# Kernel optimization log

Measured on AMD Instinct MI355X. Metric: run time of the kernel, lower is better.

The kernel has to match this reference:

```python
import jax, jax.numpy as jnp
import numpy as np

N = 8000          # num_nodes
DEG = 8           # avg out-degree of random road graph
B = 32            # batch size
INPUT_DIM = 2
UNITS = 64        # rnn_units
K = 2             # max_diffusion_step
NUM_SUPPORTS = 2  # dual_random_walk


def _spmm(rows, cols, vals, x):
    # sparse @ dense: y[r] += vals * x[c] for each coo entry (r, c)
    return jax.ops.segment_sum(vals[:, None] * x[cols], rows, num_segments=N)


def _gconv(inputs, state, supports, W, b):
    # Chebyshev-style diffusion conv, faithful to GCONV.forward layout
    Bsz = inputs.shape[0]
    x = jnp.concatenate([inputs.reshape(Bsz, N, -1), state.reshape(Bsz, N, -1)], axis=2)
    F = x.shape[2]                                   # input_dim + units
    x0 = jnp.transpose(x, (1, 2, 0)).reshape(N, F * Bsz)
    xs = [x0]
    for rows, cols, vals in supports:
        x1 = _spmm(rows, cols, vals, x0)
        xs.append(x1)
        xk2, xk1 = x0, x1
        for _ in range(2, K + 1):
            x2 = 2.0 * _spmm(rows, cols, vals, xk1) - xk2
            xs.append(x2)
            xk2, xk1 = xk1, x2
    M = len(xs)                                      # num_matrices = 2*K+1
    xc = jnp.stack(xs).reshape(M, N, F, Bsz)
    xc = jnp.transpose(xc, (3, 1, 2, 0)).reshape(Bsz * N, F * M)
    out = xc @ W + b
    return out.reshape(Bsz, N * W.shape[1])


def setup_inputs() -> dict:
    rng = np.random.default_rng(0)
    rows = np.repeat(np.arange(N, dtype=np.int32), DEG)
    cols = rng.integers(0, N, size=N * DEG).astype(np.int32)
    vals = rng.uniform(0.5, 1.5, size=N * DEG).astype(np.float32)
    # random-walk normalization: rw(A) = D^-1 A ; supports are rw(A).T and rw(A.T).T
    rsum = np.zeros(N, np.float32); np.add.at(rsum, rows, vals)
    csum = np.zeros(N, np.float32); np.add.at(csum, cols, vals)
    rinv = np.where(rsum > 0, 1.0 / np.maximum(rsum, 1e-12), 0.0).astype(np.float32)
    cinv = np.where(csum > 0, 1.0 / np.maximum(csum, 1e-12), 0.0).astype(np.float32)
    # support0 = (D^-1 A)^T: entry (cols[i], rows[i]) = vals[i] * rinv[rows[i]]
    s0_rows, s0_cols, s0_vals = cols, rows, (vals * rinv[rows]).astype(np.float32)
    # support1 = (D_T^-1 A^T)^T: entry (rows[i], cols[i]) = vals[i] * cinv[cols[i]]
    s1_rows, s1_cols, s1_vals = rows, cols, (vals * cinv[cols]).astype(np.float32)

    key = jax.random.key(0)
    k1, k2, k3, k4 = jax.random.split(key, 4)
    F = INPUT_DIM + UNITS
    M = NUM_SUPPORTS * K + 1
    xavier = lambda k, shape: jax.random.normal(k, shape, jnp.float32) * np.float32(np.sqrt(2.0 / (shape[0] + shape[1])))
    W_ru = xavier(k1, (F * M, 2 * UNITS))
    b_ru = jnp.ones((2 * UNITS,), jnp.float32)    # bias_start=1.0
    W_c = xavier(k2, (F * M, UNITS))
    b_c = jnp.zeros((UNITS,), jnp.float32)        # bias_start=0.0
    inputs = jax.random.normal(k3, (B, N * INPUT_DIM), jnp.float32)
    hx = jax.random.normal(k4, (B, N * UNITS), jnp.float32)
    return {
        "inputs": inputs, "hx": hx,
        "W_ru": W_ru, "b_ru": b_ru, "W_c": W_c, "b_c": b_c,
        "s0_rows": jnp.asarray(s0_rows), "s0_cols": jnp.asarray(s0_cols), "s0_vals": jnp.asarray(s0_vals),
        "s1_rows": jnp.asarray(s1_rows), "s1_cols": jnp.asarray(s1_cols), "s1_vals": jnp.asarray(s1_vals),
    }


def reference(inputs, hx, W_ru, b_ru, W_c, b_c,
              s0_rows, s0_cols, s0_vals, s1_rows, s1_cols, s1_vals):
    supports = [(s0_rows, s0_cols, s0_vals), (s1_rows, s1_cols, s1_vals)]
    value = jax.nn.sigmoid(_gconv(inputs, hx, supports, W_ru, b_ru))
    value = value.reshape(-1, N, 2 * UNITS)
    r = value[..., :UNITS].reshape(-1, N * UNITS)
    u = value[..., UNITS:].reshape(-1, N * UNITS)
    c = jnp.tanh(_gconv(inputs, r * hx, supports, W_c, b_c))
    return u * hx + (1.0 - u) * c
```

## Files before the change

### kernel.cpp

```cpp
#include <hip/hip_runtime.h>
#include <stdint.h>

typedef unsigned short u16;
typedef unsigned int   u32;

typedef __attribute__((ext_vector_type(8))) short bf16x8;
typedef __attribute__((ext_vector_type(4))) float f32x4;

#define NNODES 8000
#define BSZ    32
#define UNITS  64
#define EDG    64000
#define ROWCH  288
#define NODECH 1440
#define NODEU16 11520
#define KLIN   384
#define NSTEPS 12
#define HXROW  512000
#define INROW  16000

__device__ __forceinline__ u32 f2bf(float f){
    u32 u = __float_as_uint(f);
    return (u + 0x7FFFu + ((u >> 16) & 1u)) >> 16;
}
__device__ __forceinline__ float bfu(u16 s){ return __uint_as_float(((u32)s) << 16); }
__device__ __forceinline__ float lo16(u32 u){ return __uint_as_float(u << 16); }
__device__ __forceinline__ float hi16(u32 u){ return __uint_as_float(u & 0xFFFF0000u); }
__device__ __forceinline__ float sigm(float x){ return 1.f / (1.f + __expf(-x)); }

#define GLDS(gsrc, ldst) \
    __builtin_amdgcn_global_load_lds((const __attribute__((address_space(1))) void*)(gsrc), \
                                     (__attribute__((address_space(3))) void*)(ldst), 16, 0, 0)

__global__ void hist_k(const int* __restrict__ rows, int* __restrict__ counts){
    int e = blockIdx.x * 256 + threadIdx.x;
    if (e < EDG) atomicAdd(&counts[rows[e]], 1);
}

__global__ __launch_bounds__(256) void scan_k(const int* __restrict__ counts,
                                              int* __restrict__ row_ptr,
                                              int* __restrict__ cursor){
    __shared__ int part[256];
    int t = threadIdx.x;
    int s = 0;
    for (int i = 0; i < 32; ++i){ int r = t*32 + i; if (r < NNODES) s += counts[r]; }
    part[t] = s;
    __syncthreads();
    if (t == 0){
        int run = 0;
        for (int i = 0; i < 256; ++i){ int v = part[i]; part[i] = run; run += v; }
    }
    __syncthreads();
    int run = part[t];
    for (int i = 0; i < 32; ++i){
        int r = t*32 + i;
        if (r < NNODES){ row_ptr[r] = run; cursor[r] = run; run += counts[r]; }
    }
    if (t == 255) row_ptr[NNODES] = run;
}

__global__ void scatter_k(const int* __restrict__ rows, const int* __restrict__ cols,
                          const float* __restrict__ vals, int* __restrict__ cursor,
                          int* __restrict__ cs, float* __restrict__ vs){
    int e = blockIdx.x * 256 + threadIdx.x;
    if (e < EDG){
        int r = rows[e];
        int slot = atomicAdd(&cursor[r], 1);
        cs[slot] = cols[e];
        vs[slot] = vals[e];
    }
}

__global__ void prep_w_k(const float* __restrict__ W_ru, const float* __restrict__ W_c,
                         u16* __restrict__ Wt_ru, u16* __restrict__ Wt_c){
    int id = blockIdx.x * 256 + threadIdx.x;
    if (id < 128*KLIN){
        int j = id & 7;
        int cell = id >> 3;
        int col = cell & 127;
        int sq = cell >> 7;
        int kl = sq*8 + j;
        int m = kl / 72, fp = kl - m*72;
        u16 v = 0;
        if (m < 5 && fp < 66){
            float w;
            if (m == 0)      w = W_ru[(fp*5 + 0)*128 + col] - W_ru[(fp*5 + 2)*128 + col] - W_ru[(fp*5 + 4)*128 + col];
            else if (m == 2) w = 2.f * W_ru[(fp*5 + 2)*128 + col];
            else if (m == 4) w = 2.f * W_ru[(fp*5 + 4)*128 + col];
            else             w = W_ru[(fp*5 + m)*128 + col];
            v = (u16)f2bf(w);
        }
        Wt_ru[id] = v;
    }
    int id2 = id - 128*KLIN;
    if (id2 >= 0 && id2 < 64*KLIN){
        int j = id2 & 7;
        int cell = id2 >> 3;
        int col = cell & 63;
        int sq = cell >> 6;
        int kl = sq*8 + j;
        int m = kl / 72, fp = kl - m*72;
        u16 v = 0;
        if (m < 5 && fp < 66){
            float w;
            if (m == 0)      w = W_c[(fp*5 + 0)*64 + col] - W_c[(fp*5 + 2)*64 + col] - W_c[(fp*5 + 4)*64 + col];
            else if (m == 2) w = 2.f * W_c[(fp*5 + 2)*64 + col];
            else if (m == 4) w = 2.f * W_c[(fp*5 + 4)*64 + col];
            else             w = W_c[(fp*5 + m)*64 + col];
            v = (u16)f2bf(w);
        }
        Wt_c[id2] = v;
    }
}

__global__ __launch_bounds__(256) void build_x0_k(const float* __restrict__ inputs,
                                                  const float* __restrict__ hx,
                                                  u16* __restrict__ Xu){
    __shared__ float sl[32*72];
    int n = blockIdx.x, t = threadIdx.x;
    #pragma unroll
    for (int i = 0; i < 8; ++i){
        int idx = t + i*256;
        int b = idx >> 6, f = idx & 63;
        sl[b*72 + 2 + f] = hx[b*HXROW + n*64 + f];
    }
    if (t < 64){
        int b = t >> 1, d = t & 1;
        sl[b*72 + d] = inputs[b*INROW + n*2 + d];
    }
    if (t < 192){
        int b = t / 6, k = t - b*6;
        sl[b*72 + 66 + k] = 0.f;
    }
    __syncthreads();
    #pragma unroll
    for (int i = 0; i < 2; ++i){
        int j = t + i*256;
        if (j < ROWCH){
            int b = j & 31, s = j >> 5;
            const float* p = &sl[b*72 + s*8];
            uint4 o;
            o.x = f2bf(p[0]) | (f2bf(p[1]) << 16);
            o.y = f2bf(p[2]) | (f2bf(p[3]) << 16);
            o.z = f2bf(p[4]) | (f2bf(p[5]) << 16);
            o.w = f2bf(p[6]) | (f2bf(p[7]) << 16);
            ((uint4*)Xu)[(size_t)n*NODECH + j] = o;
        }
    }
}

__device__ __forceinline__ void acc8(float* a, uint4 q, float v){
    a[0] += v*lo16(q.x); a[1] += v*hi16(q.x);
    a[2] += v*lo16(q.y); a[3] += v*hi16(q.y);
    a[4] += v*lo16(q.z); a[5] += v*hi16(q.z);
    a[6] += v*lo16(q.w); a[7] += v*hi16(q.w);
}
__device__ __forceinline__ uint4 pack8(const float* a){
    uint4 o;
    o.x = f2bf(a[0]) | (f2bf(a[1]) << 16);
    o.y = f2bf(a[2]) | (f2bf(a[3]) << 16);
    o.z = f2bf(a[4]) | (f2bf(a[5]) << 16);
    o.w = f2bf(a[6]) | (f2bf(a[7]) << 16);
    return o;
}

__global__ __launch_bounds__(288) void diff1_k(u16* __restrict__ Xu,
                                               const int* __restrict__ rp,
                                               const int* __restrict__ c0, const float* __restrict__ v0,
                                               const int* __restrict__ c1, const float* __restrict__ v1){
    int t = threadIdx.x;
    if (t >= ROWCH) return;
    int n = blockIdx.x;
    const uint4* xb = (const uint4*)Xu;
    float a[8] = {0,0,0,0,0,0,0,0};
    float d[8] = {0,0,0,0,0,0,0,0};
    {
        uint4 q[8]; float vv[8];
        #pragma unroll
        for (int i = 0; i < 8; ++i){
            int c = c1[n*8 + i]; vv[i] = v1[n*8 + i];
            q[i] = xb[(size_t)c*NODECH + t];
        }
        #pragma unroll
        for (int i = 0; i < 8; ++i) acc8(d, q[i], vv[i]);
    }
    int e = rp[n], end = rp[n+1];
    for (; e + 8 <= end; e += 8){
        uint4 q[8]; float vv[8];
        #pragma unroll
        for (int i = 0; i < 8; ++i){
            int c = c0[e+i]; vv[i] = v0[e+i];
            q[i] = xb[(size_t)c*NODECH + t];
        }
        #pragma unroll
        for (int i = 0; i < 8; ++i) acc8(a, q[i], vv[i]);
    }
    for (; e < end; ++e){
        int c = c0[e]; float v = v0[e];
        acc8(a, xb[(size_t)c*NODECH + t], v);
    }
    ((uint4*)Xu)[(size_t)n*NODECH + 1*ROWCH + t] = pack8(a);
    ((uint4*)Xu)[(size_t)n*NODECH + 3*ROWCH + t] = pack8(d);
}

__global__ __launch_bounds__(288) void diff2_k(u16* __restrict__ Xu,
                                               const int* __restrict__ rp,
                                               const int* __restrict__ c0, const float* __restrict__ v0,
                                               const int* __restrict__ c1, const float* __restrict__ v1){
    int t = threadIdx.x;
    if (t >= ROWCH) return;
    int n = blockIdx.x;
    const uint4* xb = (const uint4*)Xu;
    float a[8] = {0,0,0,0,0,0,0,0};
    float d[8] = {0,0,0,0,0,0,0,0};
    {
        uint4 q[8]; float vv[8];
        #pragma unroll
        for (int i = 0; i < 8; ++i){
            int c = c1[n*8 + i]; vv[i] = v1[n*8 + i];
            q[i] = xb[(size_t)c*NODECH + 3*ROWCH + t];
        }
        #pragma unroll
        for (int i = 0; i < 8; ++i) acc8(d, q[i], vv[i]);
    }
    int e = rp[n], end = rp[n+1];
    for (; e + 8 <= end; e += 8){
        uint4 q[8]; float vv[8];
        #pragma unroll
        for (int i = 0; i < 8; ++i){
            int c = c0[e+i]; vv[i] = v0[e+i];
            q[i] = xb[(size_t)c*NODECH + 1*ROWCH + t];
        }
        #pragma unroll
        for (int i = 0; i < 8; ++i) acc8(a, q[i], vv[i]);
    }
    for (; e < end; ++e){
        int c = c0[e]; float v = v0[e];
        acc8(a, xb[(size_t)c*NODECH + 1*ROWCH + t], v);
    }
    ((uint4*)Xu)[(size_t)n*NODECH + 2*ROWCH + t] = pack8(a);
    ((uint4*)Xu)[(size_t)n*NODECH + 4*ROWCH + t] = pack8(d);
}

__global__ __launch_bounds__(1024) void gemm_ru_k(
        const u16* Xu,
        const u16* __restrict__ WtS,
        const float* __restrict__ b_ru,
        u16* __restrict__ U, u16* X0st){
    __shared__ u16 Bs[24576];
    const int t = threadIdx.x;
    const int lane = t & 63, w = t >> 6;
    const int node = blockIdx.x*16 + w;
    const int cIn = lane & 15, q = lane >> 4;
    const size_t noff = (size_t)node * NODEU16;
    const u16* Xn = Xu + noff;

    f32x4 acc[2][8];
    const f32x4 z4 = {0.f,0.f,0.f,0.f};
    #pragma unroll
    for (int rt = 0; rt < 2; ++rt)
        #pragma unroll
        for (int ct = 0; ct < 8; ++ct) acc[rt][ct] = z4;

    #pragma unroll
    for (int i = 0; i < 3; ++i)
        GLDS(WtS + (size_t)(i*1024 + t)*8, &Bs[(i*1024 + t)*8]);
    __syncthreads();

    #pragma unroll
    for (int h = 0; h < 2; ++h){
        if (h == 1){
            __syncthreads();
            #pragma unroll
            for (int i = 0; i < 3; ++i)
                GLDS(WtS + (size_t)(3072 + i*1024 + t)*8, &Bs[(i*1024 + t)*8]);
            __syncthreads();
        }
        #pragma unroll
        for (int ls = 0; ls < 6; ++ls){
            const int st = h*6 + ls;
            bf16x8 A0 = *(const bf16x8*)&Xn[(size_t)((st*4 + q)*32 + cIn)*8];
            bf16x8 A1 = *(const bf16x8*)&Xn[(size_t)((st*4 + q)*32 + 16 + cIn)*8];
            bf16x8 cb[8];
            #pragma unroll
            for (int ct = 0; ct < 8; ++ct)
                cb[ct] = *(const bf16x8*)&Bs[((ls*4 + q)*128 + ct*16 + cIn)*8];
            #pragma unroll
            for (int ct = 0; ct < 8; ++ct){
                acc[0][ct] = __builtin_amdgcn_mfma_f32_16x16x32_bf16(A0, cb[ct], acc[0][ct], 0,0,0);
                acc[1][ct] = __builtin_amdgcn_mfma_f32_16x16x32_bf16(A1, cb[ct], acc[1][ct], 0,0,0);
            }
        }
    }

    #pragma unroll
    for (int ct = 0; ct < 8; ++ct){
        int col = ct*16 + cIn;
        float bias = b_ru[col];
        #pragma unroll
        for (int rt = 0; rt < 2; ++rt){
            int b0 = rt*16 + q*4;
            f32x4 d = acc[rt][ct];
            if (ct < 4){
                int fp = 2 + col;
                int s = fp >> 3, off = fp & 7;
                #pragma unroll
                for (int i = 0; i < 4; ++i){
                    size_t idx = noff + (size_t)(s*32 + b0 + i)*8 + off;
                    float h2 = bfu(X0st[idx]);
                    float rg = sigm(d[i] + bias);
                    X0st[idx] = (u16)f2bf(rg * h2);
                }
            } else {
                uint2 pk;
                float v0 = sigm(d[0] + bias), v1 = sigm(d[1] + bias);
                float v2 = sigm(d[2] + bias), v3 = sigm(d[3] + bias);
                pk.x = f2bf(v0) | (f2bf(v1) << 16);
                pk.y = f2bf(v2) | (f2bf(v3) << 16);
                *(uint2*)&U[(size_t)node*2048 + (col - 64)*32 + b0] = pk;
            }
        }
    }
}

__global__ __launch_bounds__(1024) void gemm_c_k(
        const u16* __restrict__ Xu,
        const u16* __restrict__ WtS,
        const float* __restrict__ b_c, const float* __restrict__ hx,
        const u16* __restrict__ U, float* __restrict__ out){
    __shared__ u16 Bs[24576];
    const int t = threadIdx.x;
    const int lane = t & 63, w = t >> 6;
    const int node = blockIdx.x*16 + w;
    const int cIn = lane & 15, q = lane >> 4;
    const size_t noff = (size_t)node * NODEU16;
    const u16* Xn = Xu + noff;

    f32x4 acc[2][4];
    const f32x4 z4 = {0.f,0.f,0.f,0.f};
    #pragma unroll
    for (int rt = 0; rt < 2; ++rt)
        #pragma unroll
        for (int ct = 0; ct < 4; ++ct) acc[rt][ct] = z4;

    #pragma unroll
    for (int i = 0; i < 3; ++i)
        GLDS(WtS + (size_t)(i*1024 + t)*8, &Bs[(i*1024 + t)*8]);
    __syncthreads();

    #pragma unroll
    for (int st = 0; st < NSTEPS; ++st){
        bf16x8 A0 = *(const bf16x8*)&Xn[(size_t)((st*4 + q)*32 + cIn)*8];
        bf16x8 A1 = *(const bf16x8*)&Xn[(size_t)((st*4 + q)*32 + 16 + cIn)*8];
        bf16x8 cb[4];
        #pragma unroll
        for (int ct = 0; ct < 4; ++ct)
            cb[ct] = *(const bf16x8*)&Bs[((st*4 + q)*64 + ct*16 + cIn)*8];
        #pragma unroll
        for (int ct = 0; ct < 4; ++ct){
            acc[0][ct] = __builtin_amdgcn_mfma_f32_16x16x32_bf16(A0, cb[ct], acc[0][ct], 0,0,0);
            acc[1][ct] = __builtin_amdgcn_mfma_f32_16x16x32_bf16(A1, cb[ct], acc[1][ct], 0,0,0);
        }
    }

    #pragma unroll
    for (int ct = 0; ct < 4; ++ct){
        int col = ct*16 + cIn;
        float bias = b_c[col];
        #pragma unroll
        for (int rt = 0; rt < 2; ++rt){
            int b0 = rt*16 + q*4;
            f32x4 d = acc[rt][ct];
            uint2 up = *(const uint2*)&U[(size_t)node*2048 + col*32 + b0];
            float uu[4] = { lo16(up.x), hi16(up.x), lo16(up.y), hi16(up.y) };
            #pragma unroll
            for (int i = 0; i < 4; ++i){
                float c = tanhf(d[i] + bias);
                size_t gi = (size_t)(b0 + i)*HXROW + node*64 + col;
                float h = hx[gi];
                out[gi] = uu[i]*h + (1.f - uu[i])*c;
            }
        }
    }
}

extern "C" void kernel_launch(void* const* d_in, const int* in_sizes, int n_in,
                              void* d_out, int out_size, void* d_ws, size_t ws_size,
                              hipStream_t stream){
    const float* inputs = (const float*)d_in[0];
    const float* hx     = (const float*)d_in[1];
    const float* W_ru   = (const float*)d_in[2];
    const float* b_ru   = (const float*)d_in[3];
    const float* W_c    = (const float*)d_in[4];
    const float* b_c    = (const float*)d_in[5];
    const int*   s0r    = (const int*)d_in[6];
    const int*   s0c    = (const int*)d_in[7];
    const float* s0v    = (const float*)d_in[8];
    const int*   s1c    = (const int*)d_in[10];
    const float* s1v    = (const float*)d_in[11];
    float* out = (float*)d_out;

    char* ws = (char*)d_ws;
    size_t off = 0;
    auto alloc = [&](size_t bytes) -> char* {
        char* p = ws + off;
        off += (bytes + 255) & ~(size_t)255;
        return p;
    };
    const size_t XU_BYTES = (size_t)NNODES * NODEU16 * 2;
    u16* Xu   = (u16*)alloc(XU_BYTES + 4096);
    u16* U    = (u16*)alloc((size_t)NNODES*2048*2);
    u16* WtRU = (u16*)alloc((size_t)128*KLIN*2);
    u16* WtC  = (u16*)alloc((size_t)64*KLIN*2);
    int* counts  = (int*)alloc((size_t)NNODES*4);
    int* row_ptr = (int*)alloc((size_t)(NNODES+1)*4);
    int* cursor  = (int*)alloc((size_t)NNODES*4);
    int*   cols_s = (int*)alloc((size_t)EDG*4);
    float* vals_s = (float*)alloc((size_t)EDG*4);
    (void)ws_size; (void)in_sizes; (void)n_in; (void)out_size;

    hipMemsetAsync(counts, 0, (size_t)NNODES*4, stream);
    hipMemsetAsync((char*)Xu + XU_BYTES, 0, 4096, stream);
    hist_k<<<250, 256, 0, stream>>>(s0r, counts);
    scan_k<<<1, 256, 0, stream>>>(counts, row_ptr, cursor);
    scatter_k<<<250, 256, 0, stream>>>(s0r, s0c, s0v, cursor, cols_s, vals_s);

    prep_w_k<<<288, 256, 0, stream>>>(W_ru, W_c, WtRU, WtC);
    build_x0_k<<<NNODES, 256, 0, stream>>>(inputs, hx, Xu);

    diff1_k<<<NNODES, 288, 0, stream>>>(Xu, row_ptr, cols_s, vals_s, s1c, s1v);
    diff2_k<<<NNODES, 288, 0, stream>>>(Xu, row_ptr, cols_s, vals_s, s1c, s1v);

    gemm_ru_k<<<NNODES/16, 1024, 0, stream>>>(Xu, WtRU, b_ru, U, Xu);

    diff1_k<<<NNODES, 288, 0, stream>>>(Xu, row_ptr, cols_s, vals_s, s1c, s1v);
    diff2_k<<<NNODES, 288, 0, stream>>>(Xu, row_ptr, cols_s, vals_s, s1c, s1v);

    gemm_c_k<<<NNODES/16, 1024, 0, stream>>>(Xu, WtC, b_c, hx, U, out);
}
```

Measured before the change: 670.6 us.

## Transpose GEMM MFMA operands so epilogues emit contiguous vectorized stores

Swaps the A and B operands of the MFMA so each lane holds four consecutive output columns for one batch row instead of four batch rows for one column. The feature order in X0 is permuted (hidden state first, inputs last) and the weight prep is remapped to match, so the r*h update, U, hx and out accesses become 8- or 16-byte vector loads and stores. Bias moves into shared memory. This targets the scattered scalar global traffic in the epilogues, at the cost of touching layout in several kernels consistently.

```diff
diff --git a/kernel.cpp b/kernel.cpp
--- a/kernel.cpp
+++ b/kernel.cpp
@@ -83,11 +83,12 @@
         int m = kl / 72, fp = kl - m*72;
         u16 v = 0;
         if (m < 5 && fp < 66){
+            int of = (fp < 64) ? (fp + 2) : (fp - 64);
             float w;
-            if (m == 0)      w = W_ru[(fp*5 + 0)*128 + col] - W_ru[(fp*5 + 2)*128 + col] - W_ru[(fp*5 + 4)*128 + col];
-            else if (m == 2) w = 2.f * W_ru[(fp*5 + 2)*128 + col];
-            else if (m == 4) w = 2.f * W_ru[(fp*5 + 4)*128 + col];
-            else             w = W_ru[(fp*5 + m)*128 + col];
+            if (m == 0)      w = W_ru[(of*5 + 0)*128 + col] - W_ru[(of*5 + 2)*128 + col] - W_ru[(of*5 + 4)*128 + col];
+            else if (m == 2) w = 2.f * W_ru[(of*5 + 2)*128 + col];
+            else if (m == 4) w = 2.f * W_ru[(of*5 + 4)*128 + col];
+            else             w = W_ru[(of*5 + m)*128 + col];
             v = (u16)f2bf(w);
         }
         Wt_ru[id] = v;
@@ -102,11 +103,12 @@
         int m = kl / 72, fp = kl - m*72;
         u16 v = 0;
         if (m < 5 && fp < 66){
+            int of = (fp < 64) ? (fp + 2) : (fp - 64);
             float w;
-            if (m == 0)      w = W_c[(fp*5 + 0)*64 + col] - W_c[(fp*5 + 2)*64 + col] - W_c[(fp*5 + 4)*64 + col];
-            else if (m == 2) w = 2.f * W_c[(fp*5 + 2)*64 + col];
-            else if (m == 4) w = 2.f * W_c[(fp*5 + 4)*64 + col];
-            else             w = W_c[(fp*5 + m)*64 + col];
+            if (m == 0)      w = W_c[(of*5 + 0)*64 + col] - W_c[(of*5 + 2)*64 + col] - W_c[(of*5 + 4)*64 + col];
+            else if (m == 2) w = 2.f * W_c[(of*5 + 2)*64 + col];
+            else if (m == 4) w = 2.f * W_c[(of*5 + 4)*64 + col];
+            else             w = W_c[(of*5 + m)*64 + col];
             v = (u16)f2bf(w);
         }
         Wt_c[id2] = v;
@@ -122,11 +124,11 @@
     for (int i = 0; i < 8; ++i){
         int idx = t + i*256;
         int b = idx >> 6, f = idx & 63;
-        sl[b*72 + 2 + f] = hx[b*HXROW + n*64 + f];
+        sl[b*72 + f] = hx[b*HXROW + n*64 + f];
     }
     if (t < 64){
         int b = t >> 1, d = t & 1;
-        sl[b*72 + d] = inputs[b*INROW + n*2 + d];
+        sl[b*72 + 64 + d] = inputs[b*INROW + n*2 + d];
     }
     if (t < 192){
         int b = t / 6, k = t - b*6;
@@ -248,6 +250,7 @@
         const float* __restrict__ b_ru,
         u16* __restrict__ U, u16* X0st){
     __shared__ u16 Bs[24576];
+    __shared__ float biasL[128];
     const int t = threadIdx.x;
     const int lane = t & 63, w = t >> 6;
     const int node = blockIdx.x*16 + w;
@@ -255,13 +258,14 @@
     const size_t noff = (size_t)node * NODEU16;
     const u16* Xn = Xu + noff;
 
-    f32x4 acc[2][8];
+    f32x4 acc[8][2];
     const f32x4 z4 = {0.f,0.f,0.f,0.f};
     #pragma unroll
-    for (int rt = 0; rt < 2; ++rt)
-        #pragma unroll
-        for (int ct = 0; ct < 8; ++ct) acc[rt][ct] = z4;
-
+    for (int mt = 0; mt < 8; ++mt)
+        #pragma unroll
+        for (int nt = 0; nt < 2; ++nt) acc[mt][nt] = z4;
+
+    if (t < 128) biasL[t] = b_ru[t];
     #pragma unroll
     for (int i = 0; i < 3; ++i)
         GLDS(WtS + (size_t)(i*1024 + t)*8, &Bs[(i*1024 + t)*8]);
@@ -283,41 +287,40 @@
             bf16x8 A1 = *(const bf16x8*)&Xn[(size_t)((st*4 + q)*32 + 16 + cIn)*8];
             bf16x8 cb[8];
             #pragma unroll
-            for (int ct = 0; ct < 8; ++ct)
-                cb[ct] = *(const bf16x8*)&Bs[((ls*4 + q)*128 + ct*16 + cIn)*8];
+            for (int mt = 0; mt < 8; ++mt)
+                cb[mt] = *(const bf16x8*)&Bs[((ls*4 + q)*128 + mt*16 + cIn)*8];
             #pragma unroll
-            for (int ct = 0; ct < 8; ++ct){
-                acc[0][ct] = __builtin_amdgcn_mfma_f32_16x16x32_bf16(A0, cb[ct], acc[0][ct], 0,0,0);
-                acc[1][ct] = __builtin_amdgcn_mfma_f32_16x16x32_bf16(A1, cb[ct], acc[1][ct], 0,0,0);
+            for (int mt = 0; mt < 8; ++mt){
+                acc[mt][0] = __builtin_amdgcn_mfma_f32_16x16x32_bf16(cb[mt], A0, acc[mt][0], 0,0,0);
+                acc[mt][1] = __builtin_amdgcn_mfma_f32_16x16x32_bf16(cb[mt], A1, acc[mt][1], 0,0,0);
             }
         }
     }
 
     #pragma unroll
-    for (int ct = 0; ct < 8; ++ct){
-        int col = ct*16 + cIn;
-        float bias = b_ru[col];
-        #pragma unroll
-        for (int rt = 0; rt < 2; ++rt){
-            int b0 = rt*16 + q*4;
-            f32x4 d = acc[rt][ct];
-            if (ct < 4){
-                int fp = 2 + col;
-                int s = fp >> 3, off = fp & 7;
-                #pragma unroll
-                for (int i = 0; i < 4; ++i){
-                    size_t idx = noff + (size_t)(s*32 + b0 + i)*8 + off;
-                    float h2 = bfu(X0st[idx]);
-                    float rg = sigm(d[i] + bias);
-                    X0st[idx] = (u16)f2bf(rg * h2);
-                }
+    for (int mt = 0; mt < 8; ++mt){
+        const int wc0 = mt*16 + q*4;
+        f32x4 b4 = *(const f32x4*)&biasL[wc0];
+        #pragma unroll
+        for (int nt = 0; nt < 2; ++nt){
+            const int b = nt*16 + cIn;
+            f32x4 d = acc[mt][nt];
+            if (mt < 4){
+                size_t base = noff + (size_t)((wc0 >> 3)*32 + b)*8 + (wc0 & 7);
+                uint2 hv = *(uint2*)&X0st[base];
+                float r0 = sigm(d[0] + b4.x), r1 = sigm(d[1] + b4.y);
+                float r2 = sigm(d[2] + b4.z), r3 = sigm(d[3] + b4.w);
+                uint2 o;
+                o.x = f2bf(r0*lo16(hv.x)) | (f2bf(r1*hi16(hv.x)) << 16);
+                o.y = f2bf(r2*lo16(hv.y)) | (f2bf(r3*hi16(hv.y)) << 16);
+                *(uint2*)&X0st[base] = o;
             } else {
-                uint2 pk;
-                float v0 = sigm(d[0] + bias), v1 = sigm(d[1] + bias);
-                float v2 = sigm(d[2] + bias), v3 = sigm(d[3] + bias);
-                pk.x = f2bf(v0) | (f2bf(v1) << 16);
-                pk.y = f2bf(v2) | (f2bf(v3) << 16);
-                *(uint2*)&U[(size_t)node*2048 + (col - 64)*32 + b0] = pk;
+                float u0 = sigm(d[0] + b4.x), u1 = sigm(d[1] + b4.y);
+                float u2 = sigm(d[2] + b4.z), u3 = sigm(d[3] + b4.w);
+                uint2 o;
+                o.x = f2bf(u0) | (f2bf(u1) << 16);
+                o.y = f2bf(u2) | (f2bf(u3) << 16);
+                *(uint2*)&U[(size_t)node*2048 + b*64 + (wc0 - 64)] = o;
             }
         }
     }
@@ -329,6 +332,7 @@
         const float* __restrict__ b_c, const float* __restrict__ hx,
         const u16* __restrict__ U, float* __restrict__ out){
     __shared__ u16 Bs[24576];
+    __shared__ float biasL[64];
     const int t = threadIdx.x;
     const int lane = t & 63, w = t >> 6;
     const int node = blockIdx.x*16 + w;
@@ -336,13 +340,14 @@
     const size_t noff = (size_t)node * NODEU16;
     const u16* Xn = Xu + noff;
 
-    f32x4 acc[2][4];
+    f32x4 acc[4][2];
     const f32x4 z4 = {0.f,0.f,0.f,0.f};
     #pragma unroll
-    for (int rt = 0; rt < 2; ++rt)
-        #pragma unroll
-        for (int ct = 0; ct < 4; ++ct) acc[rt][ct] = z4;
-
+    for (int mt = 0; mt < 4; ++mt)
+        #pragma unroll
+        for (int nt = 0; nt < 2; ++nt) acc[mt][nt] = z4;
+
+    if (t < 64) biasL[t] = b_c[t];
     #pragma unroll
     for (int i = 0; i < 3; ++i)
         GLDS(WtS + (size_t)(i*1024 + t)*8, &Bs[(i*1024 + t)*8]);
@@ -354,32 +359,33 @@
         bf16x8 A1 = *(const bf16x8*)&Xn[(size_t)((st*4 + q)*32 + 16 + cIn)*8];
         bf16x8 cb[4];
         #pragma unroll
-        for (int ct = 0; ct < 4; ++ct)
-            cb[ct] = *(const bf16x8*)&Bs[((st*4 + q)*64 + ct*16 + cIn)*8];
-        #pragma unroll
-        for (int ct = 0; ct < 4; ++ct){
-            acc[0][ct] = __builtin_amdgcn_mfma_f32_16x16x32_bf16(A0, cb[ct], acc[0][ct], 0,0,0);
-            acc[1][ct] = __builtin_amdgcn_mfma_f32_16x16x32_bf16(A1, cb[ct], acc[1][ct], 0,0,0);
-        }
-    }
-
-    #pragma unroll
-    for (int ct = 0; ct < 4; ++ct){
-        int col = ct*16 + cIn;
-        float bias = b_c[col];
-        #pragma unroll
-        for (int rt = 0; rt < 2; ++rt){
-            int b0 = rt*16 + q*4;
-            f32x4 d = acc[rt][ct];
-            uint2 up = *(const uint2*)&U[(size_t)node*2048 + col*32 + b0];
-            float uu[4] = { lo16(up.x), hi16(up.x), lo16(up.y), hi16(up.y) };
-            #pragma unroll
-            for (int i = 0; i < 4; ++i){
-                float c = tanhf(d[i] + bias);
-                size_t gi = (size_t)(b0 + i)*HXROW + node*64 + col;
-                float h = hx[gi];
-                out[gi] = uu[i]*h + (1.f - uu[i])*c;
-            }
+        for (int mt = 0; mt < 4; ++mt)
+            cb[mt] = *(const bf16x8*)&Bs[((st*4 + q)*64 + mt*16 + cIn)*8];
+        #pragma unroll
+        for (int mt = 0; mt < 4; ++mt){
+            acc[mt][0] = __builtin_amdgcn_mfma_f32_16x16x32_bf16(cb[mt], A0, acc[mt][0], 0,0,0);
+            acc[mt][1] = __builtin_amdgcn_mfma_f32_16x16x32_bf16(cb[mt], A1, acc[mt][1], 0,0,0);
+        }
+    }
+
+    #pragma unroll
+    for (int mt = 0; mt < 4; ++mt){
+        const int wc0 = mt*16 + q*4;
+        f32x4 b4 = *(const f32x4*)&biasL[wc0];
+        #pragma unroll
+        for (int nt = 0; nt < 2; ++nt){
+            const int b = nt*16 + cIn;
+            f32x4 d = acc[mt][nt];
+            uint2 up = *(const uint2*)&U[(size_t)node*2048 + b*64 + wc0];
+            float u0 = lo16(up.x), u1 = hi16(up.x), u2 = lo16(up.y), u3 = hi16(up.y);
+            const size_t gi = (size_t)b*HXROW + node*64 + wc0;
+            f32x4 h4 = *(const f32x4*)&hx[gi];
+            f32x4 o;
+            o.x = u0*h4.x + (1.f - u0)*tanhf(d[0] + b4.x);
+            o.y = u1*h4.y + (1.f - u1)*tanhf(d[1] + b4.y);
+            o.z = u2*h4.z + (1.f - u2)*tanhf(d[2] + b4.z);
+            o.w = u3*h4.w + (1.f - u3)*tanhf(d[3] + b4.w);
+            *(f32x4*)&out[gi] = o;
         }
     }
 }
```

Result: faster. 651.9 us (median of 2 runs) (-2.8%).
